# Kernel optimization log

Measured on AMD Instinct MI355X. Metric: run time of the kernel, lower is better.

The kernel has to match this reference:

```python
import jax, jax.numpy as jnp
import numpy as np

N = 100_000   # nodes
E = 1_600_000 # edges
D = 128       # hidden/input dim
OUT = 32      # output dim
G = 512       # graphs in batch
L = 3         # conv layers


def setup_inputs() -> dict:
    key = jax.random.key(0)
    ks = jax.random.split(key, 12)
    s = 1.0 / np.sqrt(D)
    inp = {
        "x": jax.random.normal(ks[0], (N, D), jnp.float32),
        "edge_index": jax.random.randint(ks[1], (2, E), 0, N, dtype=jnp.int32),
        "batch": jnp.sort(jax.random.randint(ks[2], (N,), 0, G, dtype=jnp.int32)),
        "enc_W1": jax.random.normal(ks[3], (D, D), jnp.float32) * s,
        "enc_b1": jnp.zeros((D,), jnp.float32),
        "enc_W2": jax.random.normal(ks[4], (D, D), jnp.float32) * s,
        "enc_b2": jnp.zeros((D,), jnp.float32),
        "gcn_W": jax.random.normal(ks[5], (L, D, D), jnp.float32) * s,
        "gcn_b": jnp.zeros((L, D), jnp.float32),
        "dec_W1": jax.random.normal(ks[6], (D, D), jnp.float32) * s,
        "dec_b1": jnp.zeros((D,), jnp.float32),
        "dec_W2": jax.random.normal(ks[7], (D, OUT), jnp.float32) * s,
        "dec_b2": jnp.zeros((OUT,), jnp.float32),
        "num_graphs": G,
    }
    return inp


def reference(x, edge_index, batch, enc_W1, enc_b1, enc_W2, enc_b2,
              gcn_W, gcn_b, dec_W1, dec_b1, dec_W2, dec_b2, num_graphs):
    n = x.shape[0]
    src, dst = edge_index[0], edge_index[1]

    # ---- encoder MLP (Linear -> ReLU -> Linear -> ReLU) ----
    h = jax.nn.relu(x @ enc_W1 + enc_b1)
    h = jax.nn.relu(h @ enc_W2 + enc_b2)

    # ---- GCN normalization: D^{-1/2} (A + I) D^{-1/2}, degrees incl. self-loops ----
    deg = jax.ops.segment_sum(jnp.ones_like(src, dtype=h.dtype), dst, num_segments=n) + 1.0
    inv_sqrt = jax.lax.rsqrt(deg)           # [N]
    edge_coef = inv_sqrt[src] * inv_sqrt[dst]  # [E]
    self_coef = inv_sqrt * inv_sqrt            # [N]

    # ---- GCN conv layers ----
    for l in range(gcn_W.shape[0]):
        hw = h @ gcn_W[l]                                       # [N, D]
        msgs = hw[src] * edge_coef[:, None]                     # [E, D] gather
        agg = jax.ops.segment_sum(msgs, dst, num_segments=n)    # [N, D] scatter-add
        agg = agg + hw * self_coef[:, None]                     # self loops
        h = jax.nn.relu(agg + gcn_b[l])

    # ---- global add pool over graphs ----
    pooled = jax.ops.segment_sum(h, batch, num_segments=num_graphs)  # [G, D]

    # ---- decoder MLP ----
    out = jax.nn.relu(pooled @ dec_W1 + dec_b1)
    return out @ dec_W2 + dec_b2
```

## Files before the change

### kernel.cpp

```cpp
#include <hip/hip_runtime.h>

#define NNODES 100000
#define NEDGES 1600000
#define DIM    128
#define OUTD   32
#define NGRAPH 512
#define LDA    136

#define NBUCK2  256
#define BSHIFT  9
#define CAP     12288
#define EPB2    8192
#define SBLOCKS ((NEDGES + EPB2 - 1) / EPB2)
#define NBUILD  ((NNODES + 511) / 512)
#define FBLOCKS ((NNODES + 127) / 128)
#define AGGBLK  ((NNODES + 31) / 32)

using bf16x8 = __attribute__((ext_vector_type(8))) short;
using f32x4  = __attribute__((ext_vector_type(4))) float;
using f32x2  = __attribute__((ext_vector_type(2))) float;

__device__ __forceinline__ short f2bf(float f) {
    unsigned u = __float_as_uint(f);
    unsigned r = (u + 0x7fff + ((u >> 16) & 1)) >> 16;
    return (short)r;
}
__device__ __forceinline__ float bf2f(short s) {
    return __uint_as_float(((unsigned)(unsigned short)s) << 16);
}

__device__ __forceinline__ uint2 bf8_to_fp8(bf16x8 t) {
    float f0 = bf2f(t[0]), f1 = bf2f(t[1]), f2 = bf2f(t[2]), f3 = bf2f(t[3]);
    float f4 = bf2f(t[4]), f5 = bf2f(t[5]), f6 = bf2f(t[6]), f7 = bf2f(t[7]);
    uint2 o;
    o.x = __builtin_amdgcn_cvt_pk_fp8_f32(f0, f1, 0, false);
    o.x = __builtin_amdgcn_cvt_pk_fp8_f32(f2, f3, o.x, true);
    o.y = __builtin_amdgcn_cvt_pk_fp8_f32(f4, f5, 0, false);
    o.y = __builtin_amdgcn_cvt_pk_fp8_f32(f6, f7, o.y, true);
    return o;
}

__global__ __launch_bounds__(256) void k_prep(
    const float* __restrict__ eW1, const float* __restrict__ eW2,
    const float* __restrict__ gW, short* __restrict__ WT,
    int* __restrict__ gcur, float* __restrict__ pooled)
{
    int idx = blockIdx.x * 256 + threadIdx.x;
    if (idx < 5 * 16384) {
        int mat = idx >> 14, rem = idx & 16383;
        int k = rem >> 7, n = rem & 127;
        const float* src = (mat == 0) ? eW1 : (mat == 1) ? eW2
                                            : (gW + (size_t)(mat - 2) * 16384);
        WT[(size_t)mat * 16384 + n * DIM + k] = f2bf(src[k * DIM + n]);
    }
    if (idx < NBUCK2) gcur[idx] = idx * CAP;
    if (idx < NGRAPH * DIM) pooled[idx] = 0.f;
}

__global__ __launch_bounds__(512) void k_scatter(
    const int* __restrict__ src, const int* __restrict__ dst,
    int* __restrict__ gcur, unsigned* __restrict__ tmp)
{
    __shared__ unsigned short rnk[EPB2];
    __shared__ int h[NBUCK2];
    __shared__ int gbase[NBUCK2];
    const int tid  = threadIdx.x;
    const int base = blockIdx.x * EPB2;
    if (tid < NBUCK2) h[tid] = 0;
    __syncthreads();
    #pragma unroll
    for (int it = 0; it < EPB2 / 512; ++it) {
        int e = base + it * 512 + tid;
        if (e < NEDGES) {
            int b = dst[e] >> BSHIFT;
            rnk[it * 512 + tid] = (unsigned short)atomicAdd(&h[b], 1);
        }
    }
    __syncthreads();
    if (tid < NBUCK2 && h[tid] > 0)
        gbase[tid] = atomicAdd(&gcur[tid], h[tid]);
    __syncthreads();
    #pragma unroll
    for (int it = 0; it < EPB2 / 512; ++it) {
        int e = base + it * 512 + tid;
        if (e < NEDGES) {
            int d = dst[e], sv = src[e];
            int b = d >> BSHIFT;
            int pos = gbase[b] + rnk[it * 512 + tid];
            if (pos < (b + 1) * CAP)
                tmp[pos] = (unsigned)sv | ((unsigned)(d & 511) << 17);
        }
    }
}

__global__ __launch_bounds__(512) void k_build(
    const unsigned* __restrict__ tmp, const int* __restrict__ gcur,
    int* __restrict__ row_off, int* __restrict__ cntA,
    float* __restrict__ inv, int* __restrict__ col)
{
    __shared__ int hist[512], sc[512], lcur[512];
    const int tid   = threadIdx.x;
    const int b     = blockIdx.x;
    const int tbase = b * CAP;
    const int cnt_b = min(gcur[b] - tbase, CAP);
    hist[tid] = 0;
    __syncthreads();
    for (int i = tid; i < cnt_b; i += 512)
        atomicAdd(&hist[(tmp[tbase + i] >> 17) & 511], 1);
    __syncthreads();
    const int hv = hist[tid];
    sc[tid] = hv;
    __syncthreads();
    for (int off = 1; off < 512; off <<= 1) {
        int t = (tid >= off) ? sc[tid - off] : 0;
        __syncthreads();
        sc[tid] += t;
        __syncthreads();
    }
    const int start = tbase + sc[tid] - hv;
    lcur[tid] = start;
    const int node = b * 512 + tid;
    if (node < NNODES) {
        row_off[node] = start;
        cntA[node]    = hv;
        inv[node]     = rsqrtf((float)hv + 1.0f);
    }
    __syncthreads();
    for (int i = tid; i < cnt_b; i += 512) {
        unsigned t = tmp[tbase + i];
        int pos = atomicAdd(&lcur[(t >> 17) & 511], 1);
        col[pos] = (int)(t & 0x1FFFFu);
    }
}

__global__ __launch_bounds__(512, 4) void k_enc(
    const float* __restrict__ x, const short* __restrict__ WT,
    const float* __restrict__ b1, const float* __restrict__ b2,
    const float* __restrict__ inv, unsigned char* __restrict__ g8, int M)
{
    __shared__ short As[128 * LDA];
    __shared__ short Bs[128 * LDA];

    const int tid = threadIdx.x;
    const int m0  = blockIdx.x * 128;

    #pragma unroll
    for (int i = 0; i < 4; ++i) {
        int u = tid + i * 512;
        int row = u >> 4, uc = (u & 15) << 3;
        int gr = min(m0 + row, M - 1);
        const float4* sp = (const float4*)(x + (size_t)gr * DIM + uc);
        float4 f0 = sp[0], f1 = sp[1];
        short t8[8] = { f2bf(f0.x), f2bf(f0.y), f2bf(f0.z), f2bf(f0.w),
                        f2bf(f1.x), f2bf(f1.y), f2bf(f1.z), f2bf(f1.w) };
        *(bf16x8*)&As[row * LDA + uc] = *(bf16x8*)t8;
    }

    const int wave = tid >> 6, lane = tid & 63;
    const int ml = lane & 15, quad = lane >> 4;
    const int w16 = wave * 16;

    #pragma unroll
    for (int mat = 0; mat < 3; ++mat) {
        if (mat > 0) __syncthreads();
        #pragma unroll
        for (int i = 0; i < 4; ++i) {
            int u = tid + i * 512;
            int n = u >> 4, kc = (u & 15) << 3;
            *(bf16x8*)&Bs[n * LDA + kc] =
                *(const bf16x8*)(WT + (size_t)mat * 16384 + n * DIM + kc);
        }
        __syncthreads();

        f32x4 acc[8] = {};
        #pragma unroll
        for (int kk = 0; kk < 4; ++kk) {
            const int k0 = kk * 32 + quad * 8;
            bf16x8 a = *(bf16x8*)&As[(w16 + ml) * LDA + k0];
            #pragma unroll
            for (int ni = 0; ni < 8; ++ni) {
                bf16x8 b = *(bf16x8*)&Bs[(ni * 16 + ml) * LDA + k0];
                acc[ni] = __builtin_amdgcn_mfma_f32_16x16x32_bf16(a, b, acc[ni], 0, 0, 0);
            }
        }
        #pragma unroll
        for (int ni = 0; ni < 8; ++ni) {
            const int colc = ni * 16 + ml;
            #pragma unroll
            for (int r = 0; r < 4; ++r) {
                const int rowl = w16 + quad * 4 + r;
                float v = acc[ni][r];
                if (mat == 0)      v = fmaxf(v + b1[colc], 0.f);
                else if (mat == 1) v = fmaxf(v + b2[colc], 0.f);
                else               v *= inv[min(m0 + rowl, M - 1)];
                As[rowl * LDA + colc] = f2bf(v);
            }
        }
    }
    __syncthreads();

    #pragma unroll
    for (int i = 0; i < 4; ++i) {
        int u = tid + i * 512;
        int row = u >> 4, uc = (u & 15) << 3;
        int gr = m0 + row;
        if (gr < M) {
            bf16x8 t = *(bf16x8*)&As[row * LDA + uc];
            *(uint2*)(g8 + (size_t)gr * DIM + uc) = bf8_to_fp8(t);
        }
    }
}

__global__ __launch_bounds__(512) void k_agg_gemm(
    const unsigned char* __restrict__ g8v, const int* __restrict__ row_off,
    const int* __restrict__ cntA, const int* __restrict__ col,
    const float* __restrict__ inv, const float* __restrict__ bias,
    const short* __restrict__ WT, unsigned char* __restrict__ g8o)
{
    __shared__ short As[32 * LDA];
    __shared__ short Bs[128 * LDA];

    const int tid = threadIdx.x;

    #pragma unroll
    for (int i = 0; i < 4; ++i) {
        int u = tid + i * 512;
        int n = u >> 4, kc = (u & 15) << 3;
        *(bf16x8*)&Bs[n * LDA + kc] = *(const bf16x8*)(WT + n * DIM + kc);
    }

    const int wave = tid >> 6, lane = tid & 63;
    const int q    = lane >> 4;
    const int sl   = lane & 15;
    const int nl   = wave * 4 + q;
    const int m0   = blockIdx.x * 32;
    const int node = m0 + nl;

    const uint2* hp = (const uint2*)g8v;
    uint2 us = hp[(size_t)node * 16 + sl];
    f32x2 p;
    float a0, a1, a2, a3, a4, a5, a6, a7;
    p = __builtin_amdgcn_cvt_pk_f32_fp8(us.x, false); a0 = p.x; a1 = p.y;
    p = __builtin_amdgcn_cvt_pk_f32_fp8(us.x, true);  a2 = p.x; a3 = p.y;
    p = __builtin_amdgcn_cvt_pk_f32_fp8(us.y, false); a4 = p.x; a5 = p.y;
    p = __builtin_amdgcn_cvt_pk_f32_fp8(us.y, true);  a6 = p.x; a7 = p.y;

    #define ACC8(v) \
        p = __builtin_amdgcn_cvt_pk_f32_fp8(v.x, false); a0 += p.x; a1 += p.y; \
        p = __builtin_amdgcn_cvt_pk_f32_fp8(v.x, true);  a2 += p.x; a3 += p.y; \
        p = __builtin_amdgcn_cvt_pk_f32_fp8(v.y, false); a4 += p.x; a5 += p.y; \
        p = __builtin_amdgcn_cvt_pk_f32_fp8(v.y, true);  a6 += p.x; a7 += p.y;

    const int s = row_off[node];
    const int e = s + cntA[node];
    int j = s;
    for (; j + 7 < e; j += 8) {
        uint2 v0 = hp[(size_t)col[j]     * 16 + sl];
        uint2 v1 = hp[(size_t)col[j + 1] * 16 + sl];
        uint2 v2 = hp[(size_t)col[j + 2] * 16 + sl];
        uint2 v3 = hp[(size_t)col[j + 3] * 16 + sl];
        uint2 v4 = hp[(size_t)col[j + 4] * 16 + sl];
        uint2 v5 = hp[(size_t)col[j + 5] * 16 + sl];
        uint2 v6 = hp[(size_t)col[j + 6] * 16 + sl];
        uint2 v7 = hp[(size_t)col[j + 7] * 16 + sl];
        ACC8(v0) ACC8(v1) ACC8(v2) ACC8(v3)
        ACC8(v4) ACC8(v5) ACC8(v6) ACC8(v7)
    }
    for (; j + 3 < e; j += 4) {
        uint2 v0 = hp[(size_t)col[j]     * 16 + sl];
        uint2 v1 = hp[(size_t)col[j + 1] * 16 + sl];
        uint2 v2 = hp[(size_t)col[j + 2] * 16 + sl];
        uint2 v3 = hp[(size_t)col[j + 3] * 16 + sl];
        ACC8(v0) ACC8(v1) ACC8(v2) ACC8(v3)
    }
    for (; j < e; ++j) {
        uint2 v = hp[(size_t)col[j] * 16 + sl];
        ACC8(v)
    }
    #undef ACC8

    const float scv = inv[node];
    const float4 bb0 = ((const float4*)bias)[sl * 2];
    const float4 bb1 = ((const float4*)bias)[sl * 2 + 1];
    short o[8];
    o[0] = f2bf(fmaxf(fmaf(a0, scv, bb0.x), 0.f));
    o[1] = f2bf(fmaxf(fmaf(a1, scv, bb0.y), 0.f));
    o[2] = f2bf(fmaxf(fmaf(a2, scv, bb0.z), 0.f));
    o[3] = f2bf(fmaxf(fmaf(a3, scv, bb0.w), 0.f));
    o[4] = f2bf(fmaxf(fmaf(a4, scv, bb1.x), 0.f));
    o[5] = f2bf(fmaxf(fmaf(a5, scv, bb1.y), 0.f));
    o[6] = f2bf(fmaxf(fmaf(a6, scv, bb1.z), 0.f));
    o[7] = f2bf(fmaxf(fmaf(a7, scv, bb1.w), 0.f));
    *(bf16x8*)&As[nl * LDA + sl * 8] = *(bf16x8*)o;
    __syncthreads();

    const int mh = wave >> 2;
    const int nq = wave & 3;
    f32x4 acc[2] = {};
    #pragma unroll
    for (int kk = 0; kk < 4; ++kk) {
        const int k0 = kk * 32 + q * 8;
        bf16x8 a = *(bf16x8*)&As[(mh * 16 + sl) * LDA + k0];
        #pragma unroll
        for (int ni = 0; ni < 2; ++ni) {
            bf16x8 b = *(bf16x8*)&Bs[((nq * 2 + ni) * 16 + sl) * LDA + k0];
            acc[ni] = __builtin_amdgcn_mfma_f32_16x16x32_bf16(a, b, acc[ni], 0, 0, 0);
        }
    }
    __syncthreads();

    #pragma unroll
    for (int ni = 0; ni < 2; ++ni) {
        const int colc = (nq * 2 + ni) * 16 + sl;
        #pragma unroll
        for (int r = 0; r < 4; ++r) {
            const int rowl = mh * 16 + q * 4 + r;
            As[rowl * LDA + colc] = f2bf(acc[ni][r] * inv[m0 + rowl]);
        }
    }
    __syncthreads();

    {
        int row = tid >> 4, cg = (tid & 15) << 3;
        bf16x8 t = *(bf16x8*)&As[row * LDA + cg];
        *(uint2*)(g8o + (size_t)(m0 + row) * DIM + cg) = bf8_to_fp8(t);
    }
}

__global__ __launch_bounds__(512) void k_agg_pool(
    const unsigned char* __restrict__ g8v, const int* __restrict__ row_off,
    const int* __restrict__ cntA, const int* __restrict__ col,
    const float* __restrict__ inv, const float* __restrict__ bias,
    const int* __restrict__ batch, float* __restrict__ pooled)
{
    __shared__ float Hs[32][132];
    __shared__ int sbatch[32];

    const int tid = threadIdx.x;
    const int wave = tid >> 6, lane = tid & 63;
    const int q    = lane >> 4;
    const int sl   = lane & 15;
    const int nl   = wave * 4 + q;
    const int m0   = blockIdx.x * 32;
    const int node = m0 + nl;

    if (tid < 32) sbatch[tid] = batch[m0 + tid];

    const uint2* hp = (const uint2*)g8v;
    uint2 us = hp[(size_t)node * 16 + sl];
    f32x2 p;
    float a0, a1, a2, a3, a4, a5, a6, a7;
    p = __builtin_amdgcn_cvt_pk_f32_fp8(us.x, false); a0 = p.x; a1 = p.y;
    p = __builtin_amdgcn_cvt_pk_f32_fp8(us.x, true);  a2 = p.x; a3 = p.y;
    p = __builtin_amdgcn_cvt_pk_f32_fp8(us.y, false); a4 = p.x; a5 = p.y;
    p = __builtin_amdgcn_cvt_pk_f32_fp8(us.y, true);  a6 = p.x; a7 = p.y;

    #define ACC8(v) \
        p = __builtin_amdgcn_cvt_pk_f32_fp8(v.x, false); a0 += p.x; a1 += p.y; \
        p = __builtin_amdgcn_cvt_pk_f32_fp8(v.x, true);  a2 += p.x; a3 += p.y; \
        p = __builtin_amdgcn_cvt_pk_f32_fp8(v.y, false); a4 += p.x; a5 += p.y; \
        p = __builtin_amdgcn_cvt_pk_f32_fp8(v.y, true);  a6 += p.x; a7 += p.y;

    const int s = row_off[node];
    const int e = s + cntA[node];
    int j = s;
    for (; j + 7 < e; j += 8) {
        uint2 v0 = hp[(size_t)col[j]     * 16 + sl];
        uint2 v1 = hp[(size_t)col[j + 1] * 16 + sl];
        uint2 v2 = hp[(size_t)col[j + 2] * 16 + sl];
        uint2 v3 = hp[(size_t)col[j + 3] * 16 + sl];
        uint2 v4 = hp[(size_t)col[j + 4] * 16 + sl];
        uint2 v5 = hp[(size_t)col[j + 5] * 16 + sl];
        uint2 v6 = hp[(size_t)col[j + 6] * 16 + sl];
        uint2 v7 = hp[(size_t)col[j + 7] * 16 + sl];
        ACC8(v0) ACC8(v1) ACC8(v2) ACC8(v3)
        ACC8(v4) ACC8(v5) ACC8(v6) ACC8(v7)
    }
    for (; j + 3 < e; j += 4) {
        uint2 v0 = hp[(size_t)col[j]     * 16 + sl];
        uint2 v1 = hp[(size_t)col[j + 1] * 16 + sl];
        uint2 v2 = hp[(size_t)col[j + 2] * 16 + sl];
        uint2 v3 = hp[(size_t)col[j + 3] * 16 + sl];
        ACC8(v0) ACC8(v1) ACC8(v2) ACC8(v3)
    }
    for (; j < e; ++j) {
        uint2 v = hp[(size_t)col[j] * 16 + sl];
        ACC8(v)
    }
    #undef ACC8

    const float scv = inv[node];
    const float4 bb0 = ((const float4*)bias)[sl * 2];
    const float4 bb1 = ((const float4*)bias)[sl * 2 + 1];
    float4 h0, h1;
    h0.x = fmaxf(fmaf(a0, scv, bb0.x), 0.f);
    h0.y = fmaxf(fmaf(a1, scv, bb0.y), 0.f);
    h0.z = fmaxf(fmaf(a2, scv, bb0.z), 0.f);
    h0.w = fmaxf(fmaf(a3, scv, bb0.w), 0.f);
    h1.x = fmaxf(fmaf(a4, scv, bb1.x), 0.f);
    h1.y = fmaxf(fmaf(a5, scv, bb1.y), 0.f);
    h1.z = fmaxf(fmaf(a6, scv, bb1.z), 0.f);
    h1.w = fmaxf(fmaf(a7, scv, bb1.w), 0.f);
    *(float4*)&Hs[nl][sl * 8]     = h0;
    *(float4*)&Hs[nl][sl * 8 + 4] = h1;
    __syncthreads();

    const int d   = tid & 127;
    const int grp = tid >> 7;
    float acc = 0.f;
    int cg = -1;
    #pragma unroll
    for (int i = 0; i < 8; ++i) {
        const int nn = grp * 8 + i;
        const int g  = sbatch[nn];
        if (g != cg) {
            if (cg >= 0) atomicAdd(pooled + (size_t)cg * DIM + d, acc);
            cg = g; acc = 0.f;
        }
        acc += Hs[nn][d];
    }
    atomicAdd(pooled + (size_t)cg * DIM + d, acc);
}

__global__ __launch_bounds__(512) void k_dec(
    const float* __restrict__ pooled, const float* __restrict__ W1,
    const float* __restrict__ b1, const float* __restrict__ W2,
    const float* __restrict__ b2, float* __restrict__ out)
{
    __shared__ float pbuf[8][128];
    __shared__ float tbuf[8][128];
    const int wave = threadIdx.x >> 6, lane = threadIdx.x & 63;
    const int g = blockIdx.x * 8 + wave;

    float2 pv = *(const float2*)(pooled + (size_t)g * DIM + lane * 2);
    pbuf[wave][lane * 2]     = pv.x;
    pbuf[wave][lane * 2 + 1] = pv.y;
    __syncthreads();

    float t0 = 0.f, t1 = 0.f;
    #pragma unroll 8
    for (int k = 0; k < DIM; ++k) {
        float pk = pbuf[wave][k];
        float2 w = *(const float2*)(W1 + (size_t)k * DIM + lane * 2);
        t0 = fmaf(pk, w.x, t0);
        t1 = fmaf(pk, w.y, t1);
    }
    tbuf[wave][lane * 2]     = fmaxf(t0 + b1[lane * 2],     0.f);
    tbuf[wave][lane * 2 + 1] = fmaxf(t1 + b1[lane * 2 + 1], 0.f);
    __syncthreads();

    const int c = lane & 31, hh = lane >> 5;
    float part = 0.f;
    #pragma unroll 8
    for (int kk = 0; kk < 64; ++kk) {
        int k = hh * 64 + kk;
        part = fmaf(tbuf[wave][k], W2[(size_t)k * OUTD + c], part);
    }
    float other = __shfl_xor(part, 32, 64);
    if (hh == 0)
        out[(size_t)g * OUTD + c] = part + other + b2[c];
}

extern "C" void kernel_launch(void* const* d_in, const int* in_sizes, int n_in,
                              void* d_out, int out_size, void* d_ws, size_t ws_size,
                              hipStream_t stream)
{
    const float* x      = (const float*)d_in[0];
    const int*   ei     = (const int*)d_in[1];
    const int*   batch  = (const int*)d_in[2];
    const float* enc_W1 = (const float*)d_in[3];
    const float* enc_b1 = (const float*)d_in[4];
    const float* enc_W2 = (const float*)d_in[5];
    const float* enc_b2 = (const float*)d_in[6];
    const float* gcn_W  = (const float*)d_in[7];
    const float* gcn_b  = (const float*)d_in[8];
    const float* dec_W1 = (const float*)d_in[9];
    const float* dec_b1 = (const float*)d_in[10];
    const float* dec_W2 = (const float*)d_in[11];
    const float* dec_b2 = (const float*)d_in[12];
    float* out = (float*)d_out;

    const int* src = ei;
    const int* dst = ei + NEDGES;

    char* p = (char*)d_ws;
    auto alloc = [&](size_t bytes) -> void* {
        void* r = (void*)p;
        p += (bytes + 255) & ~(size_t)255;
        return r;
    };
    unsigned char* g8a    = (unsigned char*)alloc((size_t)NNODES * DIM);
    unsigned char* g8b    = (unsigned char*)alloc((size_t)NNODES * DIM);
    float*         inv    = (float*)        alloc((size_t)NNODES * sizeof(float));
    int*           row_off= (int*)          alloc((size_t)NNODES * sizeof(int));
    int*           cntA   = (int*)          alloc((size_t)NNODES * sizeof(int));
    int*           col    = (int*)          alloc((size_t)NBUCK2 * CAP * sizeof(int));
    unsigned*      tmp    = (unsigned*)     alloc((size_t)NBUCK2 * CAP * sizeof(unsigned));
    int*           gcur   = (int*)          alloc((size_t)NBUCK2 * sizeof(int));
    short*         WT     = (short*)        alloc((size_t)5 * DIM * DIM * sizeof(short));
    float*         pooled = (float*)        alloc((size_t)NGRAPH * DIM * sizeof(float));

    k_prep   <<<(5 * 16384 + 255) / 256, 256, 0, stream>>>(enc_W1, enc_W2, gcn_W,
                                                           WT, gcur, pooled);
    k_scatter<<<SBLOCKS, 512, 0, stream>>>(src, dst, gcur, tmp);
    k_build  <<<NBUILD, 512, 0, stream>>>(tmp, gcur, row_off, cntA, inv, col);

    k_enc<<<FBLOCKS, 512, 0, stream>>>(x, WT, enc_b1, enc_b2, inv, g8a, NNODES);

    k_agg_gemm<<<AGGBLK, 512, 0, stream>>>(g8a, row_off, cntA, col, inv,
                                           gcn_b,       WT + 3 * 16384, g8b);
    k_agg_gemm<<<AGGBLK, 512, 0, stream>>>(g8b, row_off, cntA, col, inv,
                                           gcn_b + 128, WT + 4 * 16384, g8a);
    k_agg_pool<<<AGGBLK, 512, 0, stream>>>(g8a, row_off, cntA, col, inv,
                                           gcn_b + 256, batch, pooled);

    k_dec <<<NGRAPH / 8, 512, 0, stream>>>(pooled, dec_W1, dec_b1,
                                           dec_W2, dec_b2, out);
}
```

Measured before the change: 303.8 us.

## Use finer CSR build buckets and XOR-swizzled LDS in aggregation GEMM

The CSR build now uses 256-node buckets (391 buckets, smaller per-bucket capacity, 2048 edges per scatter block), which gives more parallel blocks in k_scatter and k_build. The aggregation GEMM kernel drops the padded LDS stride and instead XOR-swizzles 16-byte chunks. This cuts shared memory per block so occupancy can rise, and a launch-bounds hint asks for 8 blocks per CU. The trade-off is more global bucket atomics and a smaller overflow capacity per bucket, which could silently drop edges if a bucket gets unusually full.

```diff
diff --git a/kernel.cpp b/kernel.cpp
--- a/kernel.cpp
+++ b/kernel.cpp
@@ -7,12 +7,11 @@
 #define NGRAPH 512
 #define LDA    136
 
-#define NBUCK2  256
-#define BSHIFT  9
-#define CAP     12288
-#define EPB2    8192
+#define BSHIFT  8
+#define NBUCKR  ((NNODES + 255) / 256)
+#define CAP     6144
+#define EPB2    2048
 #define SBLOCKS ((NEDGES + EPB2 - 1) / EPB2)
-#define NBUILD  ((NNODES + 511) / 512)
 #define FBLOCKS ((NNODES + 127) / 128)
 #define AGGBLK  ((NNODES + 31) / 32)
 
@@ -53,7 +52,7 @@
                                             : (gW + (size_t)(mat - 2) * 16384);
         WT[(size_t)mat * 16384 + n * DIM + k] = f2bf(src[k * DIM + n]);
     }
-    if (idx < NBUCK2) gcur[idx] = idx * CAP;
+    if (idx < NBUCKR) gcur[idx] = idx * CAP;
     if (idx < NGRAPH * DIM) pooled[idx] = 0.f;
 }
 
@@ -62,11 +61,11 @@
     int* __restrict__ gcur, unsigned* __restrict__ tmp)
 {
     __shared__ unsigned short rnk[EPB2];
-    __shared__ int h[NBUCK2];
-    __shared__ int gbase[NBUCK2];
+    __shared__ int h[NBUCKR];
+    __shared__ int gbase[NBUCKR];
     const int tid  = threadIdx.x;
     const int base = blockIdx.x * EPB2;
-    if (tid < NBUCK2) h[tid] = 0;
+    if (tid < NBUCKR) h[tid] = 0;
     __syncthreads();
     #pragma unroll
     for (int it = 0; it < EPB2 / 512; ++it) {
@@ -77,7 +76,7 @@
         }
     }
     __syncthreads();
-    if (tid < NBUCK2 && h[tid] > 0)
+    if (tid < NBUCKR && h[tid] > 0)
         gbase[tid] = atomicAdd(&gcur[tid], h[tid]);
     __syncthreads();
     #pragma unroll
@@ -88,30 +87,30 @@
             int b = d >> BSHIFT;
             int pos = gbase[b] + rnk[it * 512 + tid];
             if (pos < (b + 1) * CAP)
-                tmp[pos] = (unsigned)sv | ((unsigned)(d & 511) << 17);
-        }
-    }
-}
-
-__global__ __launch_bounds__(512) void k_build(
+                tmp[pos] = (unsigned)sv | ((unsigned)(d & 255) << 17);
+        }
+    }
+}
+
+__global__ __launch_bounds__(256) void k_build(
     const unsigned* __restrict__ tmp, const int* __restrict__ gcur,
     int* __restrict__ row_off, int* __restrict__ cntA,
     float* __restrict__ inv, int* __restrict__ col)
 {
-    __shared__ int hist[512], sc[512], lcur[512];
+    __shared__ int hist[256], sc[256], lcur[256];
     const int tid   = threadIdx.x;
     const int b     = blockIdx.x;
     const int tbase = b * CAP;
     const int cnt_b = min(gcur[b] - tbase, CAP);
     hist[tid] = 0;
     __syncthreads();
-    for (int i = tid; i < cnt_b; i += 512)
-        atomicAdd(&hist[(tmp[tbase + i] >> 17) & 511], 1);
+    for (int i = tid; i < cnt_b; i += 256)
+        atomicAdd(&hist[(tmp[tbase + i] >> 17) & 255], 1);
     __syncthreads();
     const int hv = hist[tid];
     sc[tid] = hv;
     __syncthreads();
-    for (int off = 1; off < 512; off <<= 1) {
+    for (int off = 1; off < 256; off <<= 1) {
         int t = (tid >= off) ? sc[tid - off] : 0;
         __syncthreads();
         sc[tid] += t;
@@ -119,16 +118,16 @@
     }
     const int start = tbase + sc[tid] - hv;
     lcur[tid] = start;
-    const int node = b * 512 + tid;
+    const int node = b * 256 + tid;
     if (node < NNODES) {
         row_off[node] = start;
         cntA[node]    = hv;
         inv[node]     = rsqrtf((float)hv + 1.0f);
     }
     __syncthreads();
-    for (int i = tid; i < cnt_b; i += 512) {
+    for (int i = tid; i < cnt_b; i += 256) {
         unsigned t = tmp[tbase + i];
-        int pos = atomicAdd(&lcur[(t >> 17) & 511], 1);
+        int pos = atomicAdd(&lcur[(t >> 17) & 255], 1);
         col[pos] = (int)(t & 0x1FFFFu);
     }
 }
@@ -211,22 +210,23 @@
     }
 }
 
-__global__ __launch_bounds__(512) void k_agg_gemm(
+__global__ __launch_bounds__(512, 8) void k_agg_gemm(
     const unsigned char* __restrict__ g8v, const int* __restrict__ row_off,
     const int* __restrict__ cntA, const int* __restrict__ col,
     const float* __restrict__ inv, const float* __restrict__ bias,
     const short* __restrict__ WT, unsigned char* __restrict__ g8o)
 {
-    __shared__ short As[32 * LDA];
-    __shared__ short Bs[128 * LDA];
+    __shared__ short As[32 * 128];
+    __shared__ short Bs[128 * 128];
 
     const int tid = threadIdx.x;
 
     #pragma unroll
     for (int i = 0; i < 4; ++i) {
         int u = tid + i * 512;
-        int n = u >> 4, kc = (u & 15) << 3;
-        *(bf16x8*)&Bs[n * LDA + kc] = *(const bf16x8*)(WT + n * DIM + kc);
+        int n = u >> 4, c = u & 15;
+        *(bf16x8*)&Bs[n * 128 + ((c ^ (n & 15)) << 3)] =
+            *(const bf16x8*)(WT + n * DIM + (c << 3));
     }
 
     const int wave = tid >> 6, lane = tid & 63;
@@ -291,7 +291,7 @@
     o[5] = f2bf(fmaxf(fmaf(a5, scv, bb1.y), 0.f));
     o[6] = f2bf(fmaxf(fmaf(a6, scv, bb1.z), 0.f));
     o[7] = f2bf(fmaxf(fmaf(a7, scv, bb1.w), 0.f));
-    *(bf16x8*)&As[nl * LDA + sl * 8] = *(bf16x8*)o;
+    *(bf16x8*)&As[nl * 128 + ((sl ^ (nl & 15)) << 3)] = *(bf16x8*)o;
     __syncthreads();
 
     const int mh = wave >> 2;
@@ -299,11 +299,11 @@
     f32x4 acc[2] = {};
     #pragma unroll
     for (int kk = 0; kk < 4; ++kk) {
-        const int k0 = kk * 32 + q * 8;
-        bf16x8 a = *(bf16x8*)&As[(mh * 16 + sl) * LDA + k0];
+        const int c = kk * 4 + q;
+        bf16x8 a = *(bf16x8*)&As[(mh * 16 + sl) * 128 + ((c ^ sl) << 3)];
         #pragma unroll
         for (int ni = 0; ni < 2; ++ni) {
-            bf16x8 b = *(bf16x8*)&Bs[((nq * 2 + ni) * 16 + sl) * LDA + k0];
+            bf16x8 b = *(bf16x8*)&Bs[((nq * 2 + ni) * 16 + sl) * 128 + ((c ^ sl) << 3)];
             acc[ni] = __builtin_amdgcn_mfma_f32_16x16x32_bf16(a, b, acc[ni], 0, 0, 0);
         }
     }
@@ -312,18 +312,20 @@
     #pragma unroll
     for (int ni = 0; ni < 2; ++ni) {
         const int colc = (nq * 2 + ni) * 16 + sl;
+        const int cc   = colc >> 3, cw = colc & 7;
         #pragma unroll
         for (int r = 0; r < 4; ++r) {
             const int rowl = mh * 16 + q * 4 + r;
-            As[rowl * LDA + colc] = f2bf(acc[ni][r] * inv[m0 + rowl]);
+            As[rowl * 128 + (((cc ^ (rowl & 15)) << 3) | cw)] =
+                f2bf(acc[ni][r] * inv[m0 + rowl]);
         }
     }
     __syncthreads();
 
     {
-        int row = tid >> 4, cg = (tid & 15) << 3;
-        bf16x8 t = *(bf16x8*)&As[row * LDA + cg];
-        *(uint2*)(g8o + (size_t)(m0 + row) * DIM + cg) = bf8_to_fp8(t);
+        int row = tid >> 4, c = tid & 15;
+        bf16x8 t = *(bf16x8*)&As[row * 128 + ((c ^ (row & 15)) << 3)];
+        *(uint2*)(g8o + (size_t)(m0 + row) * DIM + (c << 3)) = bf8_to_fp8(t);
     }
 }
 
@@ -494,16 +496,16 @@
     float*         inv    = (float*)        alloc((size_t)NNODES * sizeof(float));
     int*           row_off= (int*)          alloc((size_t)NNODES * sizeof(int));
     int*           cntA   = (int*)          alloc((size_t)NNODES * sizeof(int));
-    int*           col    = (int*)          alloc((size_t)NBUCK2 * CAP * sizeof(int));
-    unsigned*      tmp    = (unsigned*)     alloc((size_t)NBUCK2 * CAP * sizeof(unsigned));
-    int*           gcur   = (int*)          alloc((size_t)NBUCK2 * sizeof(int));
+    int*           col    = (int*)          alloc((size_t)NBUCKR * CAP * sizeof(int));
+    unsigned*      tmp    = (unsigned*)     alloc((size_t)NBUCKR * CAP * sizeof(unsigned));
+    int*           gcur   = (int*)          alloc((size_t)NBUCKR * sizeof(int));
     short*         WT     = (short*)        alloc((size_t)5 * DIM * DIM * sizeof(short));
     float*         pooled = (float*)        alloc((size_t)NGRAPH * DIM * sizeof(float));
 
     k_prep   <<<(5 * 16384 + 255) / 256, 256, 0, stream>>>(enc_W1, enc_W2, gcn_W,
                                                            WT, gcur, pooled);
     k_scatter<<<SBLOCKS, 512, 0, stream>>>(src, dst, gcur, tmp);
-    k_build  <<<NBUILD, 512, 0, stream>>>(tmp, gcur, row_off, cntA, inv, col);
+    k_build  <<<NBUCKR, 256, 0, stream>>>(tmp, gcur, row_off, cntA, inv, col);
 
     k_enc<<<FBLOCKS, 512, 0, stream>>>(x, WT, enc_b1, enc_b2, inv, g8a, NNODES);
 
```

New measurement: 303.4 us. Within noise of the previous version (-0.1%).

## Swizzle shared tiles, shrink encoder tile, pre-scale column indices, pack fp8 accumulation

Applied to the files above, without the earlier changes.

Replaces padded LDS rows with an XOR-swizzled 128-wide layout in the encoder and aggregation kernels, which saves shared memory and allows higher occupancy hints (6 and 8 blocks per CU). The encoder now processes 64 rows per block with a 4x2 wave grid instead of 128 rows, and gains an extra barrier before the in-place write-back. CSR column indices are stored pre-multiplied by the row stride in bytes so gathers skip the index multiply. The fp8 accumulation uses packed float2 adds. The pre-scaled indices are 32-bit and rely on node*128 fitting in that range.

```diff
diff --git a/kernel.cpp b/kernel.cpp
--- a/kernel.cpp
+++ b/kernel.cpp
@@ -5,7 +5,6 @@
 #define DIM    128
 #define OUTD   32
 #define NGRAPH 512
-#define LDA    136
 
 #define NBUCK2  256
 #define BSHIFT  9
@@ -13,7 +12,7 @@
 #define EPB2    8192
 #define SBLOCKS ((NEDGES + EPB2 - 1) / EPB2)
 #define NBUILD  ((NNODES + 511) / 512)
-#define FBLOCKS ((NNODES + 127) / 128)
+#define EBLOCKS ((NNODES + 63) / 64)
 #define AGGBLK  ((NNODES + 31) / 32)
 
 using bf16x8 = __attribute__((ext_vector_type(8))) short;
@@ -129,36 +128,37 @@
     for (int i = tid; i < cnt_b; i += 512) {
         unsigned t = tmp[tbase + i];
         int pos = atomicAdd(&lcur[(t >> 17) & 511], 1);
-        col[pos] = (int)(t & 0x1FFFFu);
-    }
-}
-
-__global__ __launch_bounds__(512, 4) void k_enc(
+        col[pos] = (int)((t & 0x1FFFFu) << 7);
+    }
+}
+
+__global__ __launch_bounds__(512, 6) void k_enc(
     const float* __restrict__ x, const short* __restrict__ WT,
     const float* __restrict__ b1, const float* __restrict__ b2,
     const float* __restrict__ inv, unsigned char* __restrict__ g8, int M)
 {
-    __shared__ short As[128 * LDA];
-    __shared__ short Bs[128 * LDA];
+    __shared__ short As[64 * 128];
+    __shared__ short Bs[128 * 128];
 
     const int tid = threadIdx.x;
-    const int m0  = blockIdx.x * 128;
-
-    #pragma unroll
-    for (int i = 0; i < 4; ++i) {
+    const int m0  = blockIdx.x * 64;
+
+    #pragma unroll
+    for (int i = 0; i < 2; ++i) {
         int u = tid + i * 512;
-        int row = u >> 4, uc = (u & 15) << 3;
+        int row = u >> 4, c = u & 15;
         int gr = min(m0 + row, M - 1);
-        const float4* sp = (const float4*)(x + (size_t)gr * DIM + uc);
+        const float4* sp = (const float4*)(x + (size_t)gr * DIM + (c << 3));
         float4 f0 = sp[0], f1 = sp[1];
         short t8[8] = { f2bf(f0.x), f2bf(f0.y), f2bf(f0.z), f2bf(f0.w),
                         f2bf(f1.x), f2bf(f1.y), f2bf(f1.z), f2bf(f1.w) };
-        *(bf16x8*)&As[row * LDA + uc] = *(bf16x8*)t8;
+        *(bf16x8*)&As[row * 128 + ((c ^ (row & 15)) << 3)] = *(bf16x8*)t8;
     }
 
     const int wave = tid >> 6, lane = tid & 63;
     const int ml = lane & 15, quad = lane >> 4;
-    const int w16 = wave * 16;
+    const int rw = wave >> 1;
+    const int cw = wave & 1;
 
     #pragma unroll
     for (int mat = 0; mat < 3; ++mat) {
@@ -166,132 +166,141 @@
         #pragma unroll
         for (int i = 0; i < 4; ++i) {
             int u = tid + i * 512;
-            int n = u >> 4, kc = (u & 15) << 3;
-            *(bf16x8*)&Bs[n * LDA + kc] =
-                *(const bf16x8*)(WT + (size_t)mat * 16384 + n * DIM + kc);
+            int n = u >> 4, c = u & 15;
+            *(bf16x8*)&Bs[n * 128 + ((c ^ (n & 15)) << 3)] =
+                *(const bf16x8*)(WT + (size_t)mat * 16384 + n * DIM + (c << 3));
         }
         __syncthreads();
 
-        f32x4 acc[8] = {};
+        f32x4 acc[4] = {};
+        const int arow = rw * 16 + ml;
         #pragma unroll
         for (int kk = 0; kk < 4; ++kk) {
-            const int k0 = kk * 32 + quad * 8;
-            bf16x8 a = *(bf16x8*)&As[(w16 + ml) * LDA + k0];
+            const int c = kk * 4 + quad;
+            bf16x8 a = *(bf16x8*)&As[arow * 128 + ((c ^ (arow & 15)) << 3)];
             #pragma unroll
-            for (int ni = 0; ni < 8; ++ni) {
-                bf16x8 b = *(bf16x8*)&Bs[(ni * 16 + ml) * LDA + k0];
+            for (int ni = 0; ni < 4; ++ni) {
+                const int brow = (cw * 4 + ni) * 16 + ml;
+                bf16x8 b = *(bf16x8*)&Bs[brow * 128 + ((c ^ (brow & 15)) << 3)];
                 acc[ni] = __builtin_amdgcn_mfma_f32_16x16x32_bf16(a, b, acc[ni], 0, 0, 0);
             }
         }
+        __syncthreads();
+
         #pragma unroll
-        for (int ni = 0; ni < 8; ++ni) {
-            const int colc = ni * 16 + ml;
+        for (int ni = 0; ni < 4; ++ni) {
+            const int colc = cw * 64 + ni * 16 + ml;
+            const int cc = colc >> 3, w = colc & 7;
             #pragma unroll
             for (int r = 0; r < 4; ++r) {
-                const int rowl = w16 + quad * 4 + r;
+                const int rowl = rw * 16 + quad * 4 + r;
                 float v = acc[ni][r];
                 if (mat == 0)      v = fmaxf(v + b1[colc], 0.f);
                 else if (mat == 1) v = fmaxf(v + b2[colc], 0.f);
                 else               v *= inv[min(m0 + rowl, M - 1)];
-                As[rowl * LDA + colc] = f2bf(v);
+                As[rowl * 128 + (((cc ^ (rowl & 15)) << 3) | w)] = f2bf(v);
             }
         }
     }
     __syncthreads();
 
     #pragma unroll
-    for (int i = 0; i < 4; ++i) {
+    for (int i = 0; i < 2; ++i) {
         int u = tid + i * 512;
-        int row = u >> 4, uc = (u & 15) << 3;
+        int row = u >> 4, c = u & 15;
         int gr = m0 + row;
         if (gr < M) {
-            bf16x8 t = *(bf16x8*)&As[row * LDA + uc];
-            *(uint2*)(g8 + (size_t)gr * DIM + uc) = bf8_to_fp8(t);
-        }
-    }
-}
-
-__global__ __launch_bounds__(512) void k_agg_gemm(
+            bf16x8 t = *(bf16x8*)&As[row * 128 + ((c ^ (row & 15)) << 3)];
+            *(uint2*)(g8 + (size_t)gr * DIM + (c << 3)) = bf8_to_fp8(t);
+        }
+    }
+}
+
+__global__ __launch_bounds__(512, 8) void k_agg_gemm(
     const unsigned char* __restrict__ g8v, const int* __restrict__ row_off,
     const int* __restrict__ cntA, const int* __restrict__ col,
     const float* __restrict__ inv, const float* __restrict__ bias,
     const short* __restrict__ WT, unsigned char* __restrict__ g8o)
 {
-    __shared__ short As[32 * LDA];
-    __shared__ short Bs[128 * LDA];
+    __shared__ short As[32 * 128];
+    __shared__ short Bs[128 * 128];
 
     const int tid = threadIdx.x;
 
     #pragma unroll
     for (int i = 0; i < 4; ++i) {
         int u = tid + i * 512;
-        int n = u >> 4, kc = (u & 15) << 3;
-        *(bf16x8*)&Bs[n * LDA + kc] = *(const bf16x8*)(WT + n * DIM + kc);
+        int n = u >> 4, c = u & 15;
+        *(bf16x8*)&Bs[n * 128 + ((c ^ (n & 15)) << 3)] =
+            *(const bf16x8*)(WT + n * DIM + (c << 3));
     }
 
     const int wave = tid >> 6, lane = tid & 63;
     const int q    = lane >> 4;
     const int sl   = lane & 15;
+    const int sl8  = sl << 3;
     const int nl   = wave * 4 + q;
     const int m0   = blockIdx.x * 32;
     const int node = m0 + nl;
 
-    const uint2* hp = (const uint2*)g8v;
-    uint2 us = hp[(size_t)node * 16 + sl];
-    f32x2 p;
-    float a0, a1, a2, a3, a4, a5, a6, a7;
-    p = __builtin_amdgcn_cvt_pk_f32_fp8(us.x, false); a0 = p.x; a1 = p.y;
-    p = __builtin_amdgcn_cvt_pk_f32_fp8(us.x, true);  a2 = p.x; a3 = p.y;
-    p = __builtin_amdgcn_cvt_pk_f32_fp8(us.y, false); a4 = p.x; a5 = p.y;
-    p = __builtin_amdgcn_cvt_pk_f32_fp8(us.y, true);  a6 = p.x; a7 = p.y;
+    f32x2 a01, a23, a45, a67;
+    {
+        uint2 us = *(const uint2*)(g8v + (size_t)node * 128 + sl8);
+        a01 = __builtin_amdgcn_cvt_pk_f32_fp8(us.x, false);
+        a23 = __builtin_amdgcn_cvt_pk_f32_fp8(us.x, true);
+        a45 = __builtin_amdgcn_cvt_pk_f32_fp8(us.y, false);
+        a67 = __builtin_amdgcn_cvt_pk_f32_fp8(us.y, true);
+    }
 
     #define ACC8(v) \
-        p = __builtin_amdgcn_cvt_pk_f32_fp8(v.x, false); a0 += p.x; a1 += p.y; \
-        p = __builtin_amdgcn_cvt_pk_f32_fp8(v.x, true);  a2 += p.x; a3 += p.y; \
-        p = __builtin_amdgcn_cvt_pk_f32_fp8(v.y, false); a4 += p.x; a5 += p.y; \
-        p = __builtin_amdgcn_cvt_pk_f32_fp8(v.y, true);  a6 += p.x; a7 += p.y;
+        a01 += __builtin_amdgcn_cvt_pk_f32_fp8(v.x, false); \
+        a23 += __builtin_amdgcn_cvt_pk_f32_fp8(v.x, true);  \
+        a45 += __builtin_amdgcn_cvt_pk_f32_fp8(v.y, false); \
+        a67 += __builtin_amdgcn_cvt_pk_f32_fp8(v.y, true);
+    #define GLD(c) (*(const uint2*)(g8v + (size_t)(unsigned)((c) + sl8)))
 
     const int s = row_off[node];
     const int e = s + cntA[node];
     int j = s;
     for (; j + 7 < e; j += 8) {
-        uint2 v0 = hp[(size_t)col[j]     * 16 + sl];
-        uint2 v1 = hp[(size_t)col[j + 1] * 16 + sl];
-        uint2 v2 = hp[(size_t)col[j + 2] * 16 + sl];
-        uint2 v3 = hp[(size_t)col[j + 3] * 16 + sl];
-        uint2 v4 = hp[(size_t)col[j + 4] * 16 + sl];
-        uint2 v5 = hp[(size_t)col[j + 5] * 16 + sl];
-        uint2 v6 = hp[(size_t)col[j + 6] * 16 + sl];
-        uint2 v7 = hp[(size_t)col[j + 7] * 16 + sl];
+        uint2 v0 = GLD(col[j]);
+        uint2 v1 = GLD(col[j + 1]);
+        uint2 v2 = GLD(col[j + 2]);
+        uint2 v3 = GLD(col[j + 3]);
+        uint2 v4 = GLD(col[j + 4]);
+        uint2 v5 = GLD(col[j + 5]);
+        uint2 v6 = GLD(col[j + 6]);
+        uint2 v7 = GLD(col[j + 7]);
         ACC8(v0) ACC8(v1) ACC8(v2) ACC8(v3)
         ACC8(v4) ACC8(v5) ACC8(v6) ACC8(v7)
     }
     for (; j + 3 < e; j += 4) {
-        uint2 v0 = hp[(size_t)col[j]     * 16 + sl];
-        uint2 v1 = hp[(size_t)col[j + 1] * 16 + sl];
-        uint2 v2 = hp[(size_t)col[j + 2] * 16 + sl];
-        uint2 v3 = hp[(size_t)col[j + 3] * 16 + sl];
+        uint2 v0 = GLD(col[j]);
+        uint2 v1 = GLD(col[j + 1]);
+        uint2 v2 = GLD(col[j + 2]);
+        uint2 v3 = GLD(col[j + 3]);
         ACC8(v0) ACC8(v1) ACC8(v2) ACC8(v3)
     }
     for (; j < e; ++j) {
-        uint2 v = hp[(size_t)col[j] * 16 + sl];
+        uint2 v = GLD(col[j]);
         ACC8(v)
     }
     #undef ACC8
+    #undef GLD
 
     const float scv = inv[node];
     const float4 bb0 = ((const float4*)bias)[sl * 2];
     const float4 bb1 = ((const float4*)bias)[sl * 2 + 1];
     short o[8];
-    o[0] = f2bf(fmaxf(fmaf(a0, scv, bb0.x), 0.f));
-    o[1] = f2bf(fmaxf(fmaf(a1, scv, bb0.y), 0.f));
-    o[2] = f2bf(fmaxf(fmaf(a2, scv, bb0.z), 0.f));
-    o[3] = f2bf(fmaxf(fmaf(a3, scv, bb0.w), 0.f));
-    o[4] = f2bf(fmaxf(fmaf(a4, scv, bb1.x), 0.f));
-    o[5] = f2bf(fmaxf(fmaf(a5, scv, bb1.y), 0.f));
-    o[6] = f2bf(fmaxf(fmaf(a6, scv, bb1.z), 0.f));
-    o[7] = f2bf(fmaxf(fmaf(a7, scv, bb1.w), 0.f));
-    *(bf16x8*)&As[nl * LDA + sl * 8] = *(bf16x8*)o;
+    o[0] = f2bf(fmaxf(fmaf(a01[0], scv, bb0.x), 0.f));
+    o[1] = f2bf(fmaxf(fmaf(a01[1], scv, bb0.y), 0.f));
+    o[2] = f2bf(fmaxf(fmaf(a23[0], scv, bb0.z), 0.f));
+    o[3] = f2bf(fmaxf(fmaf(a23[1], scv, bb0.w), 0.f));
+    o[4] = f2bf(fmaxf(fmaf(a45[0], scv, bb1.x), 0.f));
+    o[5] = f2bf(fmaxf(fmaf(a45[1], scv, bb1.y), 0.f));
+    o[6] = f2bf(fmaxf(fmaf(a67[0], scv, bb1.z), 0.f));
+    o[7] = f2bf(fmaxf(fmaf(a67[1], scv, bb1.w), 0.f));
+    *(bf16x8*)&As[nl * 128 + ((sl ^ (nl & 15)) << 3)] = *(bf16x8*)o;
     __syncthreads();
 
     const int mh = wave >> 2;
@@ -299,11 +308,11 @@
     f32x4 acc[2] = {};
     #pragma unroll
     for (int kk = 0; kk < 4; ++kk) {
-        const int k0 = kk * 32 + q * 8;
-        bf16x8 a = *(bf16x8*)&As[(mh * 16 + sl) * LDA + k0];
+        const int c = kk * 4 + q;
+        bf16x8 a = *(bf16x8*)&As[(mh * 16 + sl) * 128 + ((c ^ sl) << 3)];
         #pragma unroll
         for (int ni = 0; ni < 2; ++ni) {
-            bf16x8 b = *(bf16x8*)&Bs[((nq * 2 + ni) * 16 + sl) * LDA + k0];
+            bf16x8 b = *(bf16x8*)&Bs[((nq * 2 + ni) * 16 + sl) * 128 + ((c ^ sl) << 3)];
             acc[ni] = __builtin_amdgcn_mfma_f32_16x16x32_bf16(a, b, acc[ni], 0, 0, 0);
         }
     }
@@ -312,18 +321,20 @@
     #pragma unroll
     for (int ni = 0; ni < 2; ++ni) {
         const int colc = (nq * 2 + ni) * 16 + sl;
+        const int cc   = colc >> 3, cw = colc & 7;
         #pragma unroll
         for (int r = 0; r < 4; ++r) {
             const int rowl = mh * 16 + q * 4 + r;
-            As[rowl * LDA + colc] = f2bf(acc[ni][r] * inv[m0 + rowl]);
+            As[rowl * 128 + (((cc ^ (rowl & 15)) << 3) | cw)] =
+                f2bf(acc[ni][r] * inv[m0 + rowl]);
         }
     }
     __syncthreads();
 
     {
-        int row = tid >> 4, cg = (tid & 15) << 3;
-        bf16x8 t = *(bf16x8*)&As[row * LDA + cg];
-        *(uint2*)(g8o + (size_t)(m0 + row) * DIM + cg) = bf8_to_fp8(t);
+        int row = tid >> 4, c = tid & 15;
+        bf16x8 t = *(bf16x8*)&As[row * 128 + ((c ^ (row & 15)) << 3)];
+        *(uint2*)(g8o + (size_t)(m0 + row) * DIM + (c << 3)) = bf8_to_fp8(t);
     }
 }
 
@@ -340,67 +351,70 @@
     const int wave = tid >> 6, lane = tid & 63;
     const int q    = lane >> 4;
     const int sl   = lane & 15;
+    const int sl8  = sl << 3;
     const int nl   = wave * 4 + q;
     const int m0   = blockIdx.x * 32;
     const int node = m0 + nl;
 
     if (tid < 32) sbatch[tid] = batch[m0 + tid];
 
-    const uint2* hp = (const uint2*)g8v;
-    uint2 us = hp[(size_t)node * 16 + sl];
-    f32x2 p;
-    float a0, a1, a2, a3, a4, a5, a6, a7;
-    p = __builtin_amdgcn_cvt_pk_f32_fp8(us.x, false); a0 = p.x; a1 = p.y;
-    p = __builtin_amdgcn_cvt_pk_f32_fp8(us.x, true);  a2 = p.x; a3 = p.y;
-    p = __builtin_amdgcn_cvt_pk_f32_fp8(us.y, false); a4 = p.x; a5 = p.y;
-    p = __builtin_amdgcn_cvt_pk_f32_fp8(us.y, true);  a6 = p.x; a7 = p.y;
+    f32x2 a01, a23, a45, a67;
+    {
+        uint2 us = *(const uint2*)(g8v + (size_t)node * 128 + sl8);
+        a01 = __builtin_amdgcn_cvt_pk_f32_fp8(us.x, false);
+        a23 = __builtin_amdgcn_cvt_pk_f32_fp8(us.x, true);
+        a45 = __builtin_amdgcn_cvt_pk_f32_fp8(us.y, false);
+        a67 = __builtin_amdgcn_cvt_pk_f32_fp8(us.y, true);
+    }
 
     #define ACC8(v) \
-        p = __builtin_amdgcn_cvt_pk_f32_fp8(v.x, false); a0 += p.x; a1 += p.y; \
-        p = __builtin_amdgcn_cvt_pk_f32_fp8(v.x, true);  a2 += p.x; a3 += p.y; \
-        p = __builtin_amdgcn_cvt_pk_f32_fp8(v.y, false); a4 += p.x; a5 += p.y; \
-        p = __builtin_amdgcn_cvt_pk_f32_fp8(v.y, true);  a6 += p.x; a7 += p.y;
+        a01 += __builtin_amdgcn_cvt_pk_f32_fp8(v.x, false); \
+        a23 += __builtin_amdgcn_cvt_pk_f32_fp8(v.x, true);  \
+        a45 += __builtin_amdgcn_cvt_pk_f32_fp8(v.y, false); \
+        a67 += __builtin_amdgcn_cvt_pk_f32_fp8(v.y, true);
+    #define GLD(c) (*(const uint2*)(g8v + (size_t)(unsigned)((c) + sl8)))
 
     const int s = row_off[node];
     const int e = s + cntA[node];
     int j = s;
     for (; j + 7 < e; j += 8) {
-        uint2 v0 = hp[(size_t)col[j]     * 16 + sl];
-        uint2 v1 = hp[(size_t)col[j + 1] * 16 + sl];
-        uint2 v2 = hp[(size_t)col[j + 2] * 16 + sl];
-        uint2 v3 = hp[(size_t)col[j + 3] * 16 + sl];
-        uint2 v4 = hp[(size_t)col[j + 4] * 16 + sl];
-        uint2 v5 = hp[(size_t)col[j + 5] * 16 + sl];
-        uint2 v6 = hp[(size_t)col[j + 6] * 16 + sl];
-        uint2 v7 = hp[(size_t)col[j + 7] * 16 + sl];
+        uint2 v0 = GLD(col[j]);
+        uint2 v1 = GLD(col[j + 1]);
+        uint2 v2 = GLD(col[j + 2]);
+        uint2 v3 = GLD(col[j + 3]);
+        uint2 v4 = GLD(col[j + 4]);
+        uint2 v5 = GLD(col[j + 5]);
+        uint2 v6 = GLD(col[j + 6]);
+        uint2 v7 = GLD(col[j + 7]);
         ACC8(v0) ACC8(v1) ACC8(v2) ACC8(v3)
         ACC8(v4) ACC8(v5) ACC8(v6) ACC8(v7)
     }
     for (; j + 3 < e; j += 4) {
-        uint2 v0 = hp[(size_t)col[j]     * 16 + sl];
-        uint2 v1 = hp[(size_t)col[j + 1] * 16 + sl];
-        uint2 v2 = hp[(size_t)col[j + 2] * 16 + sl];
-        uint2 v3 = hp[(size_t)col[j + 3] * 16 + sl];
+        uint2 v0 = GLD(col[j]);
+        uint2 v1 = GLD(col[j + 1]);
+        uint2 v2 = GLD(col[j + 2]);
+        uint2 v3 = GLD(col[j + 3]);
         ACC8(v0) ACC8(v1) ACC8(v2) ACC8(v3)
     }
     for (; j < e; ++j) {
-        uint2 v = hp[(size_t)col[j] * 16 + sl];
+        uint2 v = GLD(col[j]);
         ACC8(v)
     }
     #undef ACC8
+    #undef GLD
 
     const float scv = inv[node];
     const float4 bb0 = ((const float4*)bias)[sl * 2];
     const float4 bb1 = ((const float4*)bias)[sl * 2 + 1];
     float4 h0, h1;
-    h0.x = fmaxf(fmaf(a0, scv, bb0.x), 0.f);
-    h0.y = fmaxf(fmaf(a1, scv, bb0.y), 0.f);
-    h0.z = fmaxf(fmaf(a2, scv, bb0.z), 0.f);
-    h0.w = fmaxf(fmaf(a3, scv, bb0.w), 0.f);
-    h1.x = fmaxf(fmaf(a4, scv, bb1.x), 0.f);
-    h1.y = fmaxf(fmaf(a5, scv, bb1.y), 0.f);
-    h1.z = fmaxf(fmaf(a6, scv, bb1.z), 0.f);
-    h1.w = fmaxf(fmaf(a7, scv, bb1.w), 0.f);
+    h0.x = fmaxf(fmaf(a01[0], scv, bb0.x), 0.f);
+    h0.y = fmaxf(fmaf(a01[1], scv, bb0.y), 0.f);
+    h0.z = fmaxf(fmaf(a23[0], scv, bb0.z), 0.f);
+    h0.w = fmaxf(fmaf(a23[1], scv, bb0.w), 0.f);
+    h1.x = fmaxf(fmaf(a45[0], scv, bb1.x), 0.f);
+    h1.y = fmaxf(fmaf(a45[1], scv, bb1.y), 0.f);
+    h1.z = fmaxf(fmaf(a67[0], scv, bb1.z), 0.f);
+    h1.w = fmaxf(fmaf(a67[1], scv, bb1.w), 0.f);
     *(float4*)&Hs[nl][sl * 8]     = h0;
     *(float4*)&Hs[nl][sl * 8 + 4] = h1;
     __syncthreads();
@@ -505,7 +519,7 @@
     k_scatter<<<SBLOCKS, 512, 0, stream>>>(src, dst, gcur, tmp);
     k_build  <<<NBUILD, 512, 0, stream>>>(tmp, gcur, row_off, cntA, inv, col);
 
-    k_enc<<<FBLOCKS, 512, 0, stream>>>(x, WT, enc_b1, enc_b2, inv, g8a, NNODES);
+    k_enc<<<EBLOCKS, 512, 0, stream>>>(x, WT, enc_b1, enc_b2, inv, g8a, NNODES);
 
     k_agg_gemm<<<AGGBLK, 512, 0, stream>>>(g8a, row_off, cntA, col, inv,
                                            gcn_b,       WT + 3 * 16384, g8b);
```

Result: faster. 292.9 us (-3.6%).
